# Optimization experiments

Hardware: AMD Instinct MI355X
Metric: run time of the kernel (lower is better)

## Reference

```python
import jax, jax.numpy as jnp
import numpy as np

BATCH, SEQ_LEN, D_MODEL, STATE_DIM = 8, 4096, 512, 64
LN_EPS = 1e-5


def _hippo_log_neg_eigs(state_dim):
    A = np.zeros((state_dim, state_dim))
    for i in range(state_dim):
        for j in range(state_dim):
            if i > j:
                A[i, j] = -((2 * i + 1) ** 0.5) * ((2 * j + 1) ** 0.5)
            elif i == j:
                A[i, j] = -(i + 1)
    ev = np.sort(np.linalg.eigvals(A).real)[:state_dim]
    return np.log(-ev + 1e-06).astype(np.float32)


def setup_inputs() -> dict:
    key = jax.random.key(0)
    ks = jax.random.split(key, 8)
    d, s = D_MODEL, STATE_DIM
    return {
        "x": jax.random.normal(ks[0], (BATCH, SEQ_LEN, d), dtype=jnp.float32),
        "log_A": jnp.asarray(_hippo_log_neg_eigs(s)),
        "B": jax.random.normal(ks[1], (d, s), dtype=jnp.float32) * 0.01,
        "C": jax.random.normal(ks[2], (s, d), dtype=jnp.float32) * 0.01,
        "D": jnp.zeros((d,), dtype=jnp.float32),
        "log_dt": jnp.zeros((), dtype=jnp.float32),
        "gamma": jnp.ones((d,), dtype=jnp.float32),
        "beta": jnp.zeros((d,), dtype=jnp.float32),
        "W1": jax.random.normal(ks[3], (d, 2 * d), dtype=jnp.float32) * (1.0 / np.sqrt(d)),
        "b1": jnp.zeros((2 * d,), dtype=jnp.float32),
        "W2": jax.random.normal(ks[4], (2 * d, d), dtype=jnp.float32) * (1.0 / np.sqrt(2 * d)),
        "b2": jnp.zeros((d,), dtype=jnp.float32),
    }


def _layernorm(x, gamma, beta):
    mu = jnp.mean(x, axis=-1, keepdims=True)
    var = jnp.mean(jnp.square(x - mu), axis=-1, keepdims=True)
    return (x - mu) * jax.lax.rsqrt(var + LN_EPS) * gamma + beta


def reference(x, log_A, B, C, D, log_dt, gamma, beta, W1, b1, W2, b2):
    residual = x
    xn = _layernorm(x, gamma, beta)  # [B, L, D]

    dt = jnp.exp(log_dt)
    A_bar = jnp.exp(-jnp.exp(log_A) * dt)  # [S]

    # Precompute input projections for all timesteps, then scan the diagonal recurrence.
    xB = jnp.einsum("bld,ds->lbs", xn, B)  # [L, B, S]
    h0 = jnp.zeros((xn.shape[0], A_bar.shape[0]), dtype=xn.dtype)

    def step(h, xb_t):
        h = A_bar * h + xb_t
        return h, h

    _, hs = jax.lax.scan(step, h0, xB)  # hs: [L, B, S]

    y = jnp.einsum("lbs,sd->bld", hs, C) + xn * D  # [B, L, D]
    y = y + residual

    yn = _layernorm(y, gamma, beta)
    mlp = jax.nn.gelu(yn @ W1 + b1, approximate=False) @ W2 + b2
    return y + mlp
```

## Files before the change

### kernel.cpp

```cpp
#include <hip/hip_runtime.h>
#include <math.h>

#define BATCH 8
#define SEQL 4096
#define DMODEL 512
#define SDIM 64
#define MROWS (BATCH * SEQL)
#define LN_EPS 1e-5f

typedef __attribute__((ext_vector_type(8))) short bf16x8;
typedef __attribute__((ext_vector_type(4))) float f32x4;

__device__ __forceinline__ float wave_sum(float v) {
#pragma unroll
  for (int off = 32; off > 0; off >>= 1) v += __shfl_xor(v, off, 64);
  return v;
}

__device__ __forceinline__ unsigned short f2bf(float f) {
  unsigned int u = __float_as_uint(f);
  u += 0x7fffu + ((u >> 16) & 1u);
  return (unsigned short)(u >> 16);
}

__device__ __forceinline__ float gelu_fast(float v) {
  float s = v * 0.70710678118654752f;
  float ax = fabsf(s);
  float t = 1.0f / (1.0f + 0.3275911f * ax);
  float p = ((((1.061405429f * t - 1.453152027f) * t + 1.421413741f) * t - 0.284496736f) * t +
             0.254829592f) *
            t;
  float er = 1.0f - p * __expf(-ax * ax);
  er = copysignf(er, s);
  return 0.5f * v * (1.0f + er);
}

__device__ __forceinline__ void gl2lds16(const void* g, void* l) {
  __builtin_amdgcn_global_load_lds((const __attribute__((address_space(1))) void*)g,
                                   (__attribute__((address_space(3))) void*)l, 16, 0, 0);
}

__global__ void ln_stats_kernel(const float* __restrict__ x, float* __restrict__ mu,
                                float* __restrict__ rstd, unsigned short* __restrict__ xbf) {
  int row = blockIdx.x * 4 + (threadIdx.x >> 6);
  int lane = threadIdx.x & 63;
  const float4* xp = (const float4*)(x + (size_t)row * DMODEL);
  float4 a = xp[lane * 2];
  float4 b = xp[lane * 2 + 1];
  float s = a.x + a.y + a.z + a.w + b.x + b.y + b.z + b.w;
  float q = a.x * a.x + a.y * a.y + a.z * a.z + a.w * a.w + b.x * b.x + b.y * b.y +
            b.z * b.z + b.w * b.w;
  s = wave_sum(s);
  q = wave_sum(q);
  uint4 pk;
  pk.x = (unsigned)f2bf(a.x) | ((unsigned)f2bf(a.y) << 16);
  pk.y = (unsigned)f2bf(a.z) | ((unsigned)f2bf(a.w) << 16);
  pk.z = (unsigned)f2bf(b.x) | ((unsigned)f2bf(b.y) << 16);
  pk.w = (unsigned)f2bf(b.z) | ((unsigned)f2bf(b.w) << 16);
  ((uint4*)(xbf + (size_t)row * DMODEL))[lane] = pk;
  if (lane == 0) {
    float m = s * (1.0f / DMODEL);
    float var = q * (1.0f / DMODEL) - m * m;
    mu[row] = m;
    rstd[row] = rsqrtf(var + LN_EPS);
  }
}

__device__ __forceinline__ void transpose_body(const float* __restrict__ W,
                                               unsigned short* __restrict__ Wt, int K, int N,
                                               int bx, int by,
                                               unsigned short (*tile)[65]) {
  int k0 = by * 64, n0 = bx * 64;
  int tx = threadIdx.x & 15, ty = threadIdx.x >> 4;
#pragma unroll
  for (int p = 0; p < 4; ++p) {
    int k = p * 16 + ty;
    float4 v = *(const float4*)&W[(size_t)(k0 + k) * N + n0 + tx * 4];
    tile[tx * 4 + 0][k] = f2bf(v.x);
    tile[tx * 4 + 1][k] = f2bf(v.y);
    tile[tx * 4 + 2][k] = f2bf(v.z);
    tile[tx * 4 + 3][k] = f2bf(v.w);
  }
  __syncthreads();
#pragma unroll
  for (int p = 0; p < 4; ++p) {
    int n = p * 16 + ty;
    ushort4 o;
    o.x = tile[n][tx * 4 + 0];
    o.y = tile[n][tx * 4 + 1];
    o.z = tile[n][tx * 4 + 2];
    o.w = tile[n][tx * 4 + 3];
    *(ushort4*)&Wt[(size_t)(n0 + n) * K + k0 + tx * 4] = o;
  }
}

__global__ __launch_bounds__(256) void prep_all_kernel(
    const float* __restrict__ W1, const float* __restrict__ W2, const float* __restrict__ Cm,
    const float* __restrict__ Bm, const float* __restrict__ gamma,
    const float* __restrict__ beta, unsigned short* __restrict__ w1t,
    unsigned short* __restrict__ w2t, unsigned short* __restrict__ ctb,
    unsigned short* __restrict__ Bgt, float* __restrict__ gB, float* __restrict__ bB) {
  __shared__ unsigned short tile[64][65];
  int b = blockIdx.x;
  if (b < 128) {
    transpose_body(W1, w1t, 512, 1024, b & 15, b >> 4, tile);
  } else if (b < 256) {
    transpose_body(W2, w2t, 1024, 512, (b - 128) & 7, (b - 128) >> 3, tile);
  } else if (b < 264) {
    transpose_body(Cm, ctb, 64, 512, b - 256, 0, tile);
  } else {
    int s = (b - 264) * 4 + (threadIdx.x >> 6);
    int l = threadIdx.x & 63;
    float gs = 0.0f, bs = 0.0f;
    unsigned short tmp[8];
#pragma unroll
    for (int u = 0; u < 8; ++u) {
      int d = l * 8 + u;
      float bv = Bm[(size_t)d * SDIM + s];
      float gv = gamma[d], ev = beta[d];
      gs += gv * bv;
      bs += ev * bv;
      tmp[u] = f2bf(gv * bv);
    }
    *(ushort4*)&Bgt[(size_t)s * DMODEL + l * 8] = make_ushort4(tmp[0], tmp[1], tmp[2], tmp[3]);
    *(ushort4*)&Bgt[(size_t)s * DMODEL + l * 8 + 4] =
        make_ushort4(tmp[4], tmp[5], tmp[6], tmp[7]);
    gs = wave_sum(gs);
    bs = wave_sum(bs);
    if (l == 0) {
      gB[s] = gs;
      bB[s] = bs;
    }
  }
}

__global__ __launch_bounds__(256) void xb_mfma_kernel(
    const unsigned short* __restrict__ xbf, const unsigned short* __restrict__ Bgt,
    const float* __restrict__ mu, const float* __restrict__ rstd, const float* __restrict__ gB,
    const float* __restrict__ bB, float* __restrict__ xB) {
  __shared__ unsigned short As[128 * 32];
  __shared__ unsigned short Bs[64 * 32];
  const int t = threadIdx.x;
  const int wave = t >> 6, lane = t & 63;
  const int m0 = blockIdx.x * 128;
  const int wm = wave * 32;
  const int row = t >> 2, seg = t & 3;
  const int fr = lane & 15, fq = lane >> 4;
  f32x4 acc[2][4] = {};
  for (int k0 = 0; k0 < DMODEL; k0 += 32) {
    __syncthreads();
    gl2lds16(xbf + (size_t)(m0 + row) * DMODEL + k0 + seg * 8, As + (size_t)(wave * 16) * 32);
    gl2lds16(xbf + (size_t)(m0 + 64 + row) * DMODEL + k0 + seg * 8,
             As + (size_t)(64 + wave * 16) * 32);
    gl2lds16(Bgt + (size_t)row * DMODEL + k0 + seg * 8, Bs + (size_t)(wave * 16) * 32);
    __syncthreads();
#pragma unroll
    for (int i = 0; i < 2; ++i) {
      bf16x8 a = *(const bf16x8*)&As[(wm + i * 16 + fr) * 32 + fq * 8];
#pragma unroll
      for (int j = 0; j < 4; ++j) {
        bf16x8 b = *(const bf16x8*)&Bs[(j * 16 + fr) * 32 + fq * 8];
        acc[i][j] = __builtin_amdgcn_mfma_f32_16x16x32_bf16(a, b, acc[i][j], 0, 0, 0);
      }
    }
  }
#pragma unroll
  for (int i = 0; i < 2; ++i)
#pragma unroll
    for (int r = 0; r < 4; ++r) {
      const int m = m0 + wm + i * 16 + fq * 4 + r;
      const float rr = rstd[m], negmurr = -mu[m] * rstd[m];
#pragma unroll
      for (int j = 0; j < 4; ++j) {
        const int s = j * 16 + fr;
        xB[(size_t)m * SDIM + s] = rr * acc[i][j][r] + negmurr * gB[s] + bB[s];
      }
    }
}

__global__ void scan_ends_kernel(const float* __restrict__ xB, const float* __restrict__ logA,
                                 const float* __restrict__ logdt, float* __restrict__ ends) {
  int t = blockIdx.x * 128 + threadIdx.x;
  int s = t & 63;
  int c = (t >> 6) & 63;
  int b = t >> 12;
  float a = expf(-expf(logA[s]) * expf(logdt[0]));
  const float* p = xB + ((size_t)(b * SEQL + c * 64)) * SDIM + s;
  float e = 0.0f;
#pragma unroll
  for (int i = 0; i < 64; ++i) e = a * e + p[(size_t)i * SDIM];
  ends[(b * 64 + c) * 64 + s] = e;
}

__global__ void scan_fix_kernel(const float* __restrict__ logA, const float* __restrict__ logdt,
                                const float* __restrict__ ends, const float* __restrict__ xB,
                                unsigned short* __restrict__ hsb) {
  int t = blockIdx.x * 128 + threadIdx.x;
  int s = t & 63;
  int c = (t >> 6) & 63;
  int b = t >> 12;
  float a = expf(-expf(logA[s]) * expf(logdt[0]));
  float a64 = a;
#pragma unroll
  for (int i = 0; i < 6; ++i) a64 *= a64;
  float h = 0.0f;
  for (int cp = 0; cp < c; ++cp) h = a64 * h + ends[(b * 64 + cp) * 64 + s];
  const float* p = xB + ((size_t)(b * SEQL + c * 64)) * SDIM + s;
  unsigned short* q = hsb + ((size_t)(b * SEQL + c * 64)) * SDIM + s;
#pragma unroll
  for (int i = 0; i < 64; ++i) {
    h = a * h + p[(size_t)i * SDIM];
    q[(size_t)i * SDIM] = f2bf(h);
  }
}

__global__ __launch_bounds__(512, 2) void y_ln_fused_kernel(
    const unsigned short* __restrict__ hsb, const unsigned short* __restrict__ ctb,
    const float* __restrict__ x, const float* __restrict__ mu1,
    const float* __restrict__ rstd1, const float* __restrict__ gamma,
    const float* __restrict__ beta, const float* __restrict__ Dv, float* __restrict__ out,
    unsigned short* __restrict__ yn) {
  __shared__ alignas(16) unsigned short As[128 * 64];
  __shared__ alignas(16) unsigned short Bs[512 * 64];
  __shared__ float rsum[128], rsq[128];
  const int t = threadIdx.x;
  const int wid = t >> 6, lane = t & 63;
  const int m0 = blockIdx.x * 128;
  const int wm = (wid >> 2) * 64;
  const int wn = (wid & 3) * 128;
  const int fr = lane & 15, fq = lane >> 4;
  const int srow = t >> 3;
  const int ksw = ((t & 7) ^ ((t >> 3) & 7)) << 3;
  gl2lds16(hsb + (size_t)(m0 + srow) * 64 + ksw, &As[(wid * 8) * 64]);
  gl2lds16(hsb + (size_t)(m0 + 64 + srow) * 64 + ksw, &As[(64 + wid * 8) * 64]);
#pragma unroll
  for (int h = 0; h < 8; ++h)
    gl2lds16(ctb + (size_t)(h * 64 + srow) * 64 + ksw, &Bs[(h * 64 + wid * 8) * 64]);
  if (t < 128) {
    rsum[t] = 0.0f;
    rsq[t] = 0.0f;
  }
  asm volatile("s_waitcnt vmcnt(0)" ::: "memory");
  __builtin_amdgcn_s_barrier();

  f32x4 acc[4][8] = {};
#pragma unroll
  for (int s = 0; s < 2; ++s) {
    bf16x8 af[4], bf[8];
#pragma unroll
    for (int i = 0; i < 4; ++i)
      af[i] = *(const bf16x8*)&As[(wm + i * 16 + fr) * 64 + ((s * 4 + fq) ^ (fr & 7)) * 8];
#pragma unroll
    for (int j = 0; j < 8; ++j)
      bf[j] = *(const bf16x8*)&Bs[(wn + j * 16 + fr) * 64 + ((s * 4 + fq) ^ (fr & 7)) * 8];
#pragma unroll
    for (int i = 0; i < 4; ++i)
#pragma unroll
      for (int j = 0; j < 8; ++j)
        acc[i][j] = __builtin_amdgcn_mfma_f32_16x16x32_bf16(af[i], bf[j], acc[i][j], 0, 0, 0);
  }

  float ga[8], be[8], dd[8];
#pragma unroll
  for (int j = 0; j < 8; ++j) {
    const int cg = wn + j * 16 + fr;
    ga[j] = gamma[cg];
    be[j] = beta[cg];
    dd[j] = Dv[cg];
  }
  float ps[4][4], pq[4][4];
#pragma unroll
  for (int i = 0; i < 4; ++i)
#pragma unroll
    for (int r = 0; r < 4; ++r) {
      const int m = m0 + wm + i * 16 + fq * 4 + r;
      const float mu = mu1[m], rs = rstd1[m];
      float s1 = 0.0f, s2 = 0.0f;
#pragma unroll
      for (int j = 0; j < 8; ++j) {
        const int cg = wn + j * 16 + fr;
        const float xv = x[(size_t)m * DMODEL + cg];
        float yv = acc[i][j][r] + ((xv - mu) * rs * ga[j] + be[j]) * dd[j] + xv;
        out[(size_t)m * DMODEL + cg] = yv;
        acc[i][j][r] = yv;
        s1 += yv;
        s2 += yv * yv;
      }
      ps[i][r] = s1;
      pq[i][r] = s2;
    }
#pragma unroll
  for (int i = 0; i < 4; ++i)
#pragma unroll
    for (int r = 0; r < 4; ++r) {
#pragma unroll
      for (int off = 1; off < 16; off <<= 1) {
        ps[i][r] += __shfl_xor(ps[i][r], off, 64);
        pq[i][r] += __shfl_xor(pq[i][r], off, 64);
      }
    }
  if (fr == 0) {
#pragma unroll
    for (int i = 0; i < 4; ++i)
#pragma unroll
      for (int r = 0; r < 4; ++r) {
        atomicAdd(&rsum[wm + i * 16 + fq * 4 + r], ps[i][r]);
        atomicAdd(&rsq[wm + i * 16 + fq * 4 + r], pq[i][r]);
      }
  }
  __syncthreads();
#pragma unroll
  for (int i = 0; i < 4; ++i)
#pragma unroll
    for (int r = 0; r < 4; ++r) {
      const int rl = wm + i * 16 + fq * 4 + r;
      const int m = m0 + rl;
      const float mu2 = rsum[rl] * (1.0f / DMODEL);
      const float var = rsq[rl] * (1.0f / DMODEL) - mu2 * mu2;
      const float rs2 = rsqrtf(var + LN_EPS);
#pragma unroll
      for (int j = 0; j < 8; ++j) {
        const int cg = wn + j * 16 + fr;
        yn[(size_t)m * DMODEL + cg] = f2bf((acc[i][j][r] - mu2) * rs2 * ga[j] + be[j]);
      }
    }
}

template <int K, int NALL, int EPI>
__global__ __launch_bounds__(256, 2) void gemm128_kernel(
    const unsigned short* __restrict__ Am, const unsigned short* __restrict__ Bm,
    const float* __restrict__ bias, unsigned short* __restrict__ gout,
    float* __restrict__ out) {
  __shared__ alignas(16) unsigned short As[2][128 * 64];
  __shared__ alignas(16) unsigned short Bs[2][128 * 64];
  const int t = threadIdx.x;
  const int wid = t >> 6, lane = t & 63;
  const int nwg = gridDim.x * gridDim.y;
  const int orig = blockIdx.y * gridDim.x + blockIdx.x;
  const int swz = (orig & 7) * (nwg >> 3) + (orig >> 3);
  const int m0 = (swz / gridDim.x) * 128, n0 = (swz % gridDim.x) * 128;
  const int wm = (wid >> 1) * 64, wn = (wid & 1) * 64;
  const int fr = lane & 15, fq = lane >> 4;
  constexpr int NT = K / 64;
  const int srow = t >> 3;
  const int ksw = ((t & 7) ^ ((t >> 3) & 7)) << 3;

  auto stageA = [&](int bb, int kt) {
    const unsigned short* s0 = Am + (size_t)(m0 + srow) * K + kt * 64 + ksw;
#pragma unroll
    for (int q = 0; q < 4; ++q)
      gl2lds16(s0 + (size_t)(q * 32) * K, &As[bb][(q * 32 + wid * 8) * 64]);
  };
  auto stageB = [&](int bb, int kt) {
    const unsigned short* s0 = Bm + (size_t)(n0 + srow) * K + kt * 64 + ksw;
#pragma unroll
    for (int q = 0; q < 4; ++q)
      gl2lds16(s0 + (size_t)(q * 32) * K, &Bs[bb][(q * 32 + wid * 8) * 64]);
  };

  stageA(0, 0);
  stageB(0, 0);
  asm volatile("s_waitcnt vmcnt(0)" ::: "memory");
  __builtin_amdgcn_s_barrier();
  __builtin_amdgcn_sched_barrier(0);

  f32x4 acc[4][4] = {};
  for (int c = 0; c < NT; ++c) {
    const int b = c & 1;
    if (c + 1 < NT) {
      stageA(b ^ 1, c + 1);
      stageB(b ^ 1, c + 1);
    }
    bf16x8 av[2][4], bv[2][4];
#pragma unroll
    for (int s = 0; s < 2; ++s) {
#pragma unroll
      for (int i = 0; i < 4; ++i)
        av[s][i] =
            *(const bf16x8*)&As[b][(wm + i * 16 + fr) * 64 + ((s * 4 + fq) ^ (fr & 7)) * 8];
#pragma unroll
      for (int j = 0; j < 4; ++j)
        bv[s][j] =
            *(const bf16x8*)&Bs[b][(wn + j * 16 + fr) * 64 + ((s * 4 + fq) ^ (fr & 7)) * 8];
    }
    __builtin_amdgcn_s_setprio(1);
#pragma unroll
    for (int s = 0; s < 2; ++s)
#pragma unroll
      for (int i = 0; i < 4; ++i)
#pragma unroll
        for (int j = 0; j < 4; ++j)
          acc[i][j] =
              __builtin_amdgcn_mfma_f32_16x16x32_bf16(av[s][i], bv[s][j], acc[i][j], 0, 0, 0);
    __builtin_amdgcn_s_setprio(0);
    if (c + 1 < NT) {
      asm volatile("s_waitcnt vmcnt(0)" ::: "memory");
      __builtin_amdgcn_s_barrier();
      __builtin_amdgcn_sched_barrier(0);
    }
  }

#pragma unroll
  for (int i = 0; i < 4; ++i)
#pragma unroll
    for (int j = 0; j < 4; ++j) {
      const int cg = n0 + wn + j * 16 + fr;
      const float bb = bias[cg];
#pragma unroll
      for (int r = 0; r < 4; ++r) {
        const int rg = m0 + wm + i * 16 + fq * 4 + r;
        if (EPI == 0) {
          gout[(size_t)rg * NALL + cg] = f2bf(gelu_fast(acc[i][j][r] + bb));
        } else {
          const size_t off = (size_t)rg * NALL + cg;
          out[off] = out[off] + acc[i][j][r] + bb;
        }
      }
    }
}

extern "C" void kernel_launch(void* const* d_in, const int* in_sizes, int n_in, void* d_out,
                              int out_size, void* d_ws, size_t ws_size, hipStream_t stream) {
  const float* x = (const float*)d_in[0];
  const float* logA = (const float*)d_in[1];
  const float* Bm = (const float*)d_in[2];
  const float* Cm = (const float*)d_in[3];
  const float* Dv = (const float*)d_in[4];
  const float* logdt = (const float*)d_in[5];
  const float* gamma = (const float*)d_in[6];
  const float* beta = (const float*)d_in[7];
  const float* W1 = (const float*)d_in[8];
  const float* b1 = (const float*)d_in[9];
  const float* W2 = (const float*)d_in[10];
  const float* b2 = (const float*)d_in[11];
  float* out = (float*)d_out;

  char* ws = (char*)d_ws;
  float* mu1 = (float*)(ws + 0);
  float* rstd1 = (float*)(ws + 131072);
  float* ends = (float*)(ws + 262144);
  float* gB = (float*)(ws + 524288);
  float* bB = (float*)(ws + 524800);
  unsigned short* Bgt = (unsigned short*)(ws + 525312);
  unsigned short* ctb = (unsigned short*)(ws + 590848);
  unsigned short* w1t = (unsigned short*)(ws + 656384);
  unsigned short* w2t = (unsigned short*)(ws + 1704960);
  unsigned short* g = (unsigned short*)(ws + 2753536);
  unsigned short* xbf = (unsigned short*)(ws + 2753536);
  float* xB = (float*)(ws + 69862400);
  unsigned short* hsb = (unsigned short*)(ws + 78251008);
  unsigned short* yn = (unsigned short*)(ws + 82445312);

  prep_all_kernel<<<280, 256, 0, stream>>>(W1, W2, Cm, Bm, gamma, beta, w1t, w2t, ctb, Bgt, gB,
                                           bB);
  ln_stats_kernel<<<MROWS / 4, 256, 0, stream>>>(x, mu1, rstd1, xbf);
  xb_mfma_kernel<<<MROWS / 128, 256, 0, stream>>>(xbf, Bgt, mu1, rstd1, gB, bB, xB);
  scan_ends_kernel<<<256, 128, 0, stream>>>(xB, logA, logdt, ends);
  scan_fix_kernel<<<256, 128, 0, stream>>>(logA, logdt, ends, xB, hsb);
  y_ln_fused_kernel<<<MROWS / 128, 512, 0, stream>>>(hsb, ctb, x, mu1, rstd1, gamma, beta, Dv,
                                                     out, yn);
  gemm128_kernel<512, 1024, 0><<<dim3(1024 / 128, MROWS / 128), 256, 0, stream>>>(
      yn, w1t, b1, g, nullptr);
  gemm128_kernel<1024, 512, 1><<<dim3(512 / 128, MROWS / 128), 256, 0, stream>>>(
      g, w2t, b2, nullptr, out);
}
```

Measured before the change: 317.1 us.

## Fuse LN stats into xB projection and restructure y-LN kernel per-wave rows

Merges the first layernorm stats kernel with the xB MFMA projection so x is read once, converted to bf16 into a swizzled LDS tile, and multiplied against B directly from global memory. This removes the xbf round trip through global memory and one launch. The y+LN kernel now has each wave own 16 full rows across all 512 columns, so row statistics are reduced with shuffles only, with no LDS atomics or block barrier. The A operand is read straight from global. GELU's reciprocal is switched to v_rcp_f32. The trade-off is much higher register pressure from 32 accumulators per lane, and larger LDS use in lnxb.

```diff
diff --git a/kernel.cpp b/kernel.cpp
--- a/kernel.cpp
+++ b/kernel.cpp
@@ -23,10 +23,16 @@
   return (unsigned short)(u >> 16);
 }
 
+__device__ __forceinline__ float frcp(float x) {
+  float r;
+  asm("v_rcp_f32 %0, %1" : "=v"(r) : "v"(x));
+  return r;
+}
+
 __device__ __forceinline__ float gelu_fast(float v) {
   float s = v * 0.70710678118654752f;
   float ax = fabsf(s);
-  float t = 1.0f / (1.0f + 0.3275911f * ax);
+  float t = frcp(1.0f + 0.3275911f * ax);
   float p = ((((1.061405429f * t - 1.453152027f) * t + 1.421413741f) * t - 0.284496736f) * t +
              0.254829592f) *
             t;
@@ -38,32 +44,6 @@
 __device__ __forceinline__ void gl2lds16(const void* g, void* l) {
   __builtin_amdgcn_global_load_lds((const __attribute__((address_space(1))) void*)g,
                                    (__attribute__((address_space(3))) void*)l, 16, 0, 0);
-}
-
-__global__ void ln_stats_kernel(const float* __restrict__ x, float* __restrict__ mu,
-                                float* __restrict__ rstd, unsigned short* __restrict__ xbf) {
-  int row = blockIdx.x * 4 + (threadIdx.x >> 6);
-  int lane = threadIdx.x & 63;
-  const float4* xp = (const float4*)(x + (size_t)row * DMODEL);
-  float4 a = xp[lane * 2];
-  float4 b = xp[lane * 2 + 1];
-  float s = a.x + a.y + a.z + a.w + b.x + b.y + b.z + b.w;
-  float q = a.x * a.x + a.y * a.y + a.z * a.z + a.w * a.w + b.x * b.x + b.y * b.y +
-            b.z * b.z + b.w * b.w;
-  s = wave_sum(s);
-  q = wave_sum(q);
-  uint4 pk;
-  pk.x = (unsigned)f2bf(a.x) | ((unsigned)f2bf(a.y) << 16);
-  pk.y = (unsigned)f2bf(a.z) | ((unsigned)f2bf(a.w) << 16);
-  pk.z = (unsigned)f2bf(b.x) | ((unsigned)f2bf(b.y) << 16);
-  pk.w = (unsigned)f2bf(b.z) | ((unsigned)f2bf(b.w) << 16);
-  ((uint4*)(xbf + (size_t)row * DMODEL))[lane] = pk;
-  if (lane == 0) {
-    float m = s * (1.0f / DMODEL);
-    float var = q * (1.0f / DMODEL) - m * m;
-    mu[row] = m;
-    rstd[row] = rsqrtf(var + LN_EPS);
-  }
 }
 
 __device__ __forceinline__ void transpose_body(const float* __restrict__ W,
@@ -134,48 +114,72 @@
   }
 }
 
-__global__ __launch_bounds__(256) void xb_mfma_kernel(
-    const unsigned short* __restrict__ xbf, const unsigned short* __restrict__ Bgt,
-    const float* __restrict__ mu, const float* __restrict__ rstd, const float* __restrict__ gB,
-    const float* __restrict__ bB, float* __restrict__ xB) {
-  __shared__ unsigned short As[128 * 32];
-  __shared__ unsigned short Bs[64 * 32];
+__global__ __launch_bounds__(256, 2) void lnxb_kernel(
+    const float* __restrict__ x, const unsigned short* __restrict__ Bgt,
+    const float* __restrict__ gB, const float* __restrict__ bB, float* __restrict__ mu1,
+    float* __restrict__ rstd1, float* __restrict__ xB) {
+  __shared__ alignas(16) unsigned short As[64 * 512];
+  __shared__ float mu_s[64], rs_s[64];
   const int t = threadIdx.x;
-  const int wave = t >> 6, lane = t & 63;
-  const int m0 = blockIdx.x * 128;
-  const int wm = wave * 32;
-  const int row = t >> 2, seg = t & 3;
+  const int m0 = blockIdx.x * 64;
+  const int row = t >> 2, q = t & 3;
+  const float4* xp = (const float4*)(x + (size_t)(m0 + row) * DMODEL + q * 128);
+  float s1 = 0.0f, s2 = 0.0f;
+#pragma unroll
+  for (int u = 0; u < 16; ++u) {
+    float4 va = xp[2 * u], vb = xp[2 * u + 1];
+    s1 += va.x + va.y + va.z + va.w + vb.x + vb.y + vb.z + vb.w;
+    s2 += va.x * va.x + va.y * va.y + va.z * va.z + va.w * va.w + vb.x * vb.x + vb.y * vb.y +
+          vb.z * vb.z + vb.w * vb.w;
+    const int slot = q * 16 + u;
+    const int sw = (slot & ~7) | ((slot ^ row) & 7);
+    uint4 pk;
+    pk.x = (unsigned)f2bf(va.x) | ((unsigned)f2bf(va.y) << 16);
+    pk.y = (unsigned)f2bf(va.z) | ((unsigned)f2bf(va.w) << 16);
+    pk.z = (unsigned)f2bf(vb.x) | ((unsigned)f2bf(vb.y) << 16);
+    pk.w = (unsigned)f2bf(vb.z) | ((unsigned)f2bf(vb.w) << 16);
+    *(uint4*)&As[(size_t)row * 512 + sw * 8] = pk;
+  }
+  s1 += __shfl_xor(s1, 1, 64);
+  s1 += __shfl_xor(s1, 2, 64);
+  s2 += __shfl_xor(s2, 1, 64);
+  s2 += __shfl_xor(s2, 2, 64);
+  if (q == 0) {
+    float m = s1 * (1.0f / DMODEL);
+    float var = s2 * (1.0f / DMODEL) - m * m;
+    float rs = rsqrtf(var + LN_EPS);
+    mu_s[row] = m;
+    rs_s[row] = rs;
+    mu1[m0 + row] = m;
+    rstd1[m0 + row] = rs;
+  }
+  __syncthreads();
+  const int wid = t >> 6, lane = t & 63;
+  const int wm = wid * 16;
   const int fr = lane & 15, fq = lane >> 4;
-  f32x4 acc[2][4] = {};
-  for (int k0 = 0; k0 < DMODEL; k0 += 32) {
-    __syncthreads();
-    gl2lds16(xbf + (size_t)(m0 + row) * DMODEL + k0 + seg * 8, As + (size_t)(wave * 16) * 32);
-    gl2lds16(xbf + (size_t)(m0 + 64 + row) * DMODEL + k0 + seg * 8,
-             As + (size_t)(64 + wave * 16) * 32);
-    gl2lds16(Bgt + (size_t)row * DMODEL + k0 + seg * 8, Bs + (size_t)(wave * 16) * 32);
-    __syncthreads();
-#pragma unroll
-    for (int i = 0; i < 2; ++i) {
-      bf16x8 a = *(const bf16x8*)&As[(wm + i * 16 + fr) * 32 + fq * 8];
-#pragma unroll
-      for (int j = 0; j < 4; ++j) {
-        bf16x8 b = *(const bf16x8*)&Bs[(j * 16 + fr) * 32 + fq * 8];
-        acc[i][j] = __builtin_amdgcn_mfma_f32_16x16x32_bf16(a, b, acc[i][j], 0, 0, 0);
-      }
-    }
-  }
-#pragma unroll
-  for (int i = 0; i < 2; ++i)
+  const int arow = wm + fr;
+  f32x4 acc[4] = {};
+#pragma unroll
+  for (int kk = 0; kk < 16; ++kk) {
+    const int slot = kk * 4 + fq;
+    const int sw = (slot & ~7) | ((slot ^ arow) & 7);
+    bf16x8 a = *(const bf16x8*)&As[(size_t)arow * 512 + sw * 8];
+#pragma unroll
+    for (int j = 0; j < 4; ++j) {
+      bf16x8 b = *(const bf16x8*)&Bgt[(size_t)(j * 16 + fr) * DMODEL + kk * 32 + fq * 8];
+      acc[j] = __builtin_amdgcn_mfma_f32_16x16x32_bf16(a, b, acc[j], 0, 0, 0);
+    }
+  }
+#pragma unroll
+  for (int j = 0; j < 4; ++j) {
+    const int s = j * 16 + fr;
+    const float gs = gB[s], bs = bB[s];
 #pragma unroll
     for (int r = 0; r < 4; ++r) {
-      const int m = m0 + wm + i * 16 + fq * 4 + r;
-      const float rr = rstd[m], negmurr = -mu[m] * rstd[m];
-#pragma unroll
-      for (int j = 0; j < 4; ++j) {
-        const int s = j * 16 + fr;
-        xB[(size_t)m * SDIM + s] = rr * acc[i][j][r] + negmurr * gB[s] + bB[s];
-      }
-    }
+      const int ml = wm + fq * 4 + r;
+      xB[(size_t)(m0 + ml) * SDIM + s] = rs_s[ml] * acc[j][r] - mu_s[ml] * rs_s[ml] * gs + bs;
+    }
+  }
 }
 
 __global__ void scan_ends_kernel(const float* __restrict__ xB, const float* __restrict__ logA,
@@ -214,116 +218,86 @@
   }
 }
 
-__global__ __launch_bounds__(512, 2) void y_ln_fused_kernel(
+__global__ __launch_bounds__(256, 2) void y_ln_fused_kernel(
     const unsigned short* __restrict__ hsb, const unsigned short* __restrict__ ctb,
     const float* __restrict__ x, const float* __restrict__ mu1,
     const float* __restrict__ rstd1, const float* __restrict__ gamma,
     const float* __restrict__ beta, const float* __restrict__ Dv, float* __restrict__ out,
     unsigned short* __restrict__ yn) {
-  __shared__ alignas(16) unsigned short As[128 * 64];
   __shared__ alignas(16) unsigned short Bs[512 * 64];
-  __shared__ float rsum[128], rsq[128];
   const int t = threadIdx.x;
   const int wid = t >> 6, lane = t & 63;
-  const int m0 = blockIdx.x * 128;
-  const int wm = (wid >> 2) * 64;
-  const int wn = (wid & 3) * 128;
+  const int m0 = blockIdx.x * 64;
+  const int wm = wid * 16;
   const int fr = lane & 15, fq = lane >> 4;
   const int srow = t >> 3;
   const int ksw = ((t & 7) ^ ((t >> 3) & 7)) << 3;
-  gl2lds16(hsb + (size_t)(m0 + srow) * 64 + ksw, &As[(wid * 8) * 64]);
-  gl2lds16(hsb + (size_t)(m0 + 64 + srow) * 64 + ksw, &As[(64 + wid * 8) * 64]);
-#pragma unroll
-  for (int h = 0; h < 8; ++h)
-    gl2lds16(ctb + (size_t)(h * 64 + srow) * 64 + ksw, &Bs[(h * 64 + wid * 8) * 64]);
-  if (t < 128) {
-    rsum[t] = 0.0f;
-    rsq[t] = 0.0f;
-  }
+#pragma unroll
+  for (int h = 0; h < 16; ++h)
+    gl2lds16(ctb + (size_t)(h * 32 + srow) * 64 + ksw, &Bs[(h * 32 + wid * 8) * 64]);
   asm volatile("s_waitcnt vmcnt(0)" ::: "memory");
   __builtin_amdgcn_s_barrier();
 
-  f32x4 acc[4][8] = {};
-#pragma unroll
-  for (int s = 0; s < 2; ++s) {
-    bf16x8 af[4], bf[8];
-#pragma unroll
-    for (int i = 0; i < 4; ++i)
-      af[i] = *(const bf16x8*)&As[(wm + i * 16 + fr) * 64 + ((s * 4 + fq) ^ (fr & 7)) * 8];
-#pragma unroll
-    for (int j = 0; j < 8; ++j)
-      bf[j] = *(const bf16x8*)&Bs[(wn + j * 16 + fr) * 64 + ((s * 4 + fq) ^ (fr & 7)) * 8];
-#pragma unroll
-    for (int i = 0; i < 4; ++i)
-#pragma unroll
-      for (int j = 0; j < 8; ++j)
-        acc[i][j] = __builtin_amdgcn_mfma_f32_16x16x32_bf16(af[i], bf[j], acc[i][j], 0, 0, 0);
-  }
-
-  float ga[8], be[8], dd[8];
-#pragma unroll
-  for (int j = 0; j < 8; ++j) {
-    const int cg = wn + j * 16 + fr;
-    ga[j] = gamma[cg];
-    be[j] = beta[cg];
-    dd[j] = Dv[cg];
-  }
-  float ps[4][4], pq[4][4];
-#pragma unroll
-  for (int i = 0; i < 4; ++i)
+  bf16x8 a0 = *(const bf16x8*)&hsb[(size_t)(m0 + wm + fr) * 64 + fq * 8];
+  bf16x8 a1 = *(const bf16x8*)&hsb[(size_t)(m0 + wm + fr) * 64 + 32 + fq * 8];
+  f32x4 acc[32];
+#pragma unroll
+  for (int j = 0; j < 32; ++j) acc[j] = f32x4{0.f, 0.f, 0.f, 0.f};
+#pragma unroll
+  for (int j = 0; j < 32; ++j) {
+    bf16x8 b0 = *(const bf16x8*)&Bs[(j * 16 + fr) * 64 + ((fq) ^ (fr & 7)) * 8];
+    bf16x8 b1 = *(const bf16x8*)&Bs[(j * 16 + fr) * 64 + ((4 + fq) ^ (fr & 7)) * 8];
+    acc[j] = __builtin_amdgcn_mfma_f32_16x16x32_bf16(a0, b0, acc[j], 0, 0, 0);
+    acc[j] = __builtin_amdgcn_mfma_f32_16x16x32_bf16(a1, b1, acc[j], 0, 0, 0);
+  }
+
+  float mur[4], rsr[4];
+#pragma unroll
+  for (int r = 0; r < 4; ++r) {
+    const int m = m0 + wm + fq * 4 + r;
+    mur[r] = mu1[m];
+    rsr[r] = rstd1[m];
+  }
+  float s1[4] = {0.f, 0.f, 0.f, 0.f}, s2[4] = {0.f, 0.f, 0.f, 0.f};
+#pragma unroll
+  for (int j = 0; j < 32; ++j) {
+    const int cg = j * 16 + fr;
+    const float ga = gamma[cg], be = beta[cg], dd = Dv[cg];
 #pragma unroll
     for (int r = 0; r < 4; ++r) {
-      const int m = m0 + wm + i * 16 + fq * 4 + r;
-      const float mu = mu1[m], rs = rstd1[m];
-      float s1 = 0.0f, s2 = 0.0f;
-#pragma unroll
-      for (int j = 0; j < 8; ++j) {
-        const int cg = wn + j * 16 + fr;
-        const float xv = x[(size_t)m * DMODEL + cg];
-        float yv = acc[i][j][r] + ((xv - mu) * rs * ga[j] + be[j]) * dd[j] + xv;
-        out[(size_t)m * DMODEL + cg] = yv;
-        acc[i][j][r] = yv;
-        s1 += yv;
-        s2 += yv * yv;
-      }
-      ps[i][r] = s1;
-      pq[i][r] = s2;
-    }
-#pragma unroll
-  for (int i = 0; i < 4; ++i)
+      const int m = m0 + wm + fq * 4 + r;
+      const float xv = x[(size_t)m * DMODEL + cg];
+      float yv = acc[j][r] + ((xv - mur[r]) * rsr[r] * ga + be) * dd + xv;
+      out[(size_t)m * DMODEL + cg] = yv;
+      acc[j][r] = yv;
+      s1[r] += yv;
+      s2[r] += yv * yv;
+    }
+  }
+#pragma unroll
+  for (int r = 0; r < 4; ++r) {
+#pragma unroll
+    for (int off = 1; off < 16; off <<= 1) {
+      s1[r] += __shfl_xor(s1[r], off, 64);
+      s2[r] += __shfl_xor(s2[r], off, 64);
+    }
+  }
+  float mu2[4], rs2[4];
+#pragma unroll
+  for (int r = 0; r < 4; ++r) {
+    mu2[r] = s1[r] * (1.0f / DMODEL);
+    rs2[r] = rsqrtf(s2[r] * (1.0f / DMODEL) - mu2[r] * mu2[r] + LN_EPS);
+  }
+#pragma unroll
+  for (int j = 0; j < 32; ++j) {
+    const int cg = j * 16 + fr;
+    const float ga = gamma[cg], be = beta[cg];
 #pragma unroll
     for (int r = 0; r < 4; ++r) {
-#pragma unroll
-      for (int off = 1; off < 16; off <<= 1) {
-        ps[i][r] += __shfl_xor(ps[i][r], off, 64);
-        pq[i][r] += __shfl_xor(pq[i][r], off, 64);
-      }
-    }
-  if (fr == 0) {
-#pragma unroll
-    for (int i = 0; i < 4; ++i)
-#pragma unroll
-      for (int r = 0; r < 4; ++r) {
-        atomicAdd(&rsum[wm + i * 16 + fq * 4 + r], ps[i][r]);
-        atomicAdd(&rsq[wm + i * 16 + fq * 4 + r], pq[i][r]);
-      }
-  }
-  __syncthreads();
-#pragma unroll
-  for (int i = 0; i < 4; ++i)
-#pragma unroll
-    for (int r = 0; r < 4; ++r) {
-      const int rl = wm + i * 16 + fq * 4 + r;
-      const int m = m0 + rl;
-      const float mu2 = rsum[rl] * (1.0f / DMODEL);
-      const float var = rsq[rl] * (1.0f / DMODEL) - mu2 * mu2;
-      const float rs2 = rsqrtf(var + LN_EPS);
-#pragma unroll
-      for (int j = 0; j < 8; ++j) {
-        const int cg = wn + j * 16 + fr;
-        yn[(size_t)m * DMODEL + cg] = f2bf((acc[i][j][r] - mu2) * rs2 * ga[j] + be[j]);
-      }
-    }
+      const int m = m0 + wm + fq * 4 + r;
+      yn[(size_t)m * DMODEL + cg] = f2bf((acc[j][r] - mu2[r]) * rs2[r] * ga + be);
+    }
+  }
 }
 
 template <int K, int NALL, int EPI>
@@ -446,19 +420,17 @@
   unsigned short* w1t = (unsigned short*)(ws + 656384);
   unsigned short* w2t = (unsigned short*)(ws + 1704960);
   unsigned short* g = (unsigned short*)(ws + 2753536);
-  unsigned short* xbf = (unsigned short*)(ws + 2753536);
   float* xB = (float*)(ws + 69862400);
   unsigned short* hsb = (unsigned short*)(ws + 78251008);
   unsigned short* yn = (unsigned short*)(ws + 82445312);
 
   prep_all_kernel<<<280, 256, 0, stream>>>(W1, W2, Cm, Bm, gamma, beta, w1t, w2t, ctb, Bgt, gB,
                                            bB);
-  ln_stats_kernel<<<MROWS / 4, 256, 0, stream>>>(x, mu1, rstd1, xbf);
-  xb_mfma_kernel<<<MROWS / 128, 256, 0, stream>>>(xbf, Bgt, mu1, rstd1, gB, bB, xB);
+  lnxb_kernel<<<MROWS / 64, 256, 0, stream>>>(x, Bgt, gB, bB, mu1, rstd1, xB);
   scan_ends_kernel<<<256, 128, 0, stream>>>(xB, logA, logdt, ends);
   scan_fix_kernel<<<256, 128, 0, stream>>>(logA, logdt, ends, xB, hsb);
-  y_ln_fused_kernel<<<MROWS / 128, 512, 0, stream>>>(hsb, ctb, x, mu1, rstd1, gamma, beta, Dv,
-                                                     out, yn);
+  y_ln_fused_kernel<<<MROWS / 64, 256, 0, stream>>>(hsb, ctb, x, mu1, rstd1, gamma, beta, Dv,
+                                                    out, yn);
   gemm128_kernel<512, 1024, 0><<<dim3(1024 / 128, MROWS / 128), 256, 0, stream>>>(
       yn, w1t, b1, g, nullptr);
   gemm128_kernel<1024, 512, 1><<<dim3(512 / 128, MROWS / 128), 256, 0, stream>>>(
```

New measurement: 355.5 us. 1.12x slower.

## Add parallel chunk-carry prefix scan kernel and use hardware rcp in GELU

Applied to the files above, without the earlier changes.

Replaces the serial per-thread loop over preceding chunk ends in scan_fix with a separate wave-level Hillis-Steele prefix scan kernel that computes carries for all chunks. Chunk ends are stored transposed so each wave reads contiguous values. Block size for the scan kernels changes from 128 to 256 threads. GELU's division is replaced with the approximate v_rcp_f32 instruction. The trade-off is one extra kernel launch and slightly lower reciprocal precision.

```diff
diff --git a/kernel.cpp b/kernel.cpp
--- a/kernel.cpp
+++ b/kernel.cpp
@@ -23,10 +23,16 @@
   return (unsigned short)(u >> 16);
 }
 
+__device__ __forceinline__ float frcp(float x) {
+  float r;
+  asm("v_rcp_f32 %0, %1" : "=v"(r) : "v"(x));
+  return r;
+}
+
 __device__ __forceinline__ float gelu_fast(float v) {
   float s = v * 0.70710678118654752f;
   float ax = fabsf(s);
-  float t = 1.0f / (1.0f + 0.3275911f * ax);
+  float t = frcp(1.0f + 0.3275911f * ax);
   float p = ((((1.061405429f * t - 1.453152027f) * t + 1.421413741f) * t - 0.284496736f) * t +
              0.254829592f) *
             t;
@@ -179,8 +185,8 @@
 }
 
 __global__ void scan_ends_kernel(const float* __restrict__ xB, const float* __restrict__ logA,
-                                 const float* __restrict__ logdt, float* __restrict__ ends) {
-  int t = blockIdx.x * 128 + threadIdx.x;
+                                 const float* __restrict__ logdt, float* __restrict__ ends_t) {
+  int t = blockIdx.x * 256 + threadIdx.x;
   int s = t & 63;
   int c = (t >> 6) & 63;
   int b = t >> 12;
@@ -189,22 +195,42 @@
   float e = 0.0f;
 #pragma unroll
   for (int i = 0; i < 64; ++i) e = a * e + p[(size_t)i * SDIM];
-  ends[(b * 64 + c) * 64 + s] = e;
+  ends_t[((size_t)(b * 64 + s)) * 64 + c] = e;
+}
+
+__global__ void scan_prefix_kernel(const float* __restrict__ logA,
+                                   const float* __restrict__ logdt,
+                                   const float* __restrict__ ends_t,
+                                   float* __restrict__ carry_t) {
+  int wid = threadIdx.x >> 6, lane = threadIdx.x & 63;
+  int pair = blockIdx.x * 4 + wid;
+  int s = pair & 63;
+  float a = expf(-expf(logA[s]) * expf(logdt[0]));
+  float a64 = a;
+#pragma unroll
+  for (int i = 0; i < 6; ++i) a64 *= a64;
+  float x = ends_t[(size_t)pair * 64 + lane];
+  float m = a64;
+#pragma unroll
+  for (int off = 1; off < 64; off <<= 1) {
+    float y = __shfl_up(x, off, 64);
+    if (lane >= off) x += m * y;
+    m = m * m;
+  }
+  float cy = __shfl_up(x, 1, 64);
+  if (lane == 0) cy = 0.0f;
+  carry_t[(size_t)pair * 64 + lane] = cy;
 }
 
 __global__ void scan_fix_kernel(const float* __restrict__ logA, const float* __restrict__ logdt,
-                                const float* __restrict__ ends, const float* __restrict__ xB,
+                                const float* __restrict__ carry_t, const float* __restrict__ xB,
                                 unsigned short* __restrict__ hsb) {
-  int t = blockIdx.x * 128 + threadIdx.x;
+  int t = blockIdx.x * 256 + threadIdx.x;
   int s = t & 63;
   int c = (t >> 6) & 63;
   int b = t >> 12;
   float a = expf(-expf(logA[s]) * expf(logdt[0]));
-  float a64 = a;
-#pragma unroll
-  for (int i = 0; i < 6; ++i) a64 *= a64;
-  float h = 0.0f;
-  for (int cp = 0; cp < c; ++cp) h = a64 * h + ends[(b * 64 + cp) * 64 + s];
+  float h = carry_t[((size_t)(b * 64 + s)) * 64 + c];
   const float* p = xB + ((size_t)(b * SEQL + c * 64)) * SDIM + s;
   unsigned short* q = hsb + ((size_t)(b * SEQL + c * 64)) * SDIM + s;
 #pragma unroll
@@ -438,7 +464,8 @@
   char* ws = (char*)d_ws;
   float* mu1 = (float*)(ws + 0);
   float* rstd1 = (float*)(ws + 131072);
-  float* ends = (float*)(ws + 262144);
+  float* ends_t = (float*)(ws + 262144);
+  float* carry_t = (float*)(ws + 393216);
   float* gB = (float*)(ws + 524288);
   float* bB = (float*)(ws + 524800);
   unsigned short* Bgt = (unsigned short*)(ws + 525312);
@@ -455,8 +482,9 @@
                                            bB);
   ln_stats_kernel<<<MROWS / 4, 256, 0, stream>>>(x, mu1, rstd1, xbf);
   xb_mfma_kernel<<<MROWS / 128, 256, 0, stream>>>(xbf, Bgt, mu1, rstd1, gB, bB, xB);
-  scan_ends_kernel<<<256, 128, 0, stream>>>(xB, logA, logdt, ends);
-  scan_fix_kernel<<<256, 128, 0, stream>>>(logA, logdt, ends, xB, hsb);
+  scan_ends_kernel<<<128, 256, 0, stream>>>(xB, logA, logdt, ends_t);
+  scan_prefix_kernel<<<128, 256, 0, stream>>>(logA, logdt, ends_t, carry_t);
+  scan_fix_kernel<<<128, 256, 0, stream>>>(logA, logdt, carry_t, xB, hsb);
   y_ln_fused_kernel<<<MROWS / 128, 512, 0, stream>>>(hsb, ctb, x, mu1, rstd1, gamma, beta, Dv,
                                                      out, yn);
   gemm128_kernel<512, 1024, 0><<<dim3(1024 / 128, MROWS / 128), 256, 0, stream>>>(
```

Result: faster. 310.7 us (-2.0%).
